# Optimization experiments

Hardware: AMD Instinct MI355X
Metric: run time of the kernel (lower is better)

The kernel has to match this reference:

```python
import jax, jax.numpy as jnp
import numpy as np
from jax import lax

# dims: B batch, C=d_model=256, IMG=128, P=4 patch, H=W=32, L=H*W=1024
# D=d_inner=512 (ssm_ratio 2.0), N=d_state=16, R=dt_rank=16, K=4 scan directions
B, C, IMG, P = 2, 256, 128, 4
H = W = IMG // P
L = H * W
D_INNER, N, R, K = 512, 16, 16, 4


def layernorm(x, g, b, eps=1e-5):
    mu = jnp.mean(x, axis=-1, keepdims=True)
    var = jnp.var(x, axis=-1, keepdims=True)
    return (x - mu) * lax.rsqrt(var + eps) * g + b


def setup_inputs() -> dict:
    key = jax.random.key(0)
    ks = jax.random.split(key, 12)
    f = lambda i, shape, s=0.02: jax.random.normal(ks[i], shape, jnp.float32) * s
    A_init = jnp.tile(jnp.arange(1, N + 1, dtype=jnp.float32)[None, None, :], (K, D_INNER, 1))
    return {
        "x": jax.random.normal(ks[0], (B, C, IMG, IMG), jnp.float32),
        "patch_w": f(1, (C, C, P, P)),
        "patch_b": jnp.zeros((C,), jnp.float32),
        "ln_g": jnp.ones((C,), jnp.float32),
        "ln_b": jnp.zeros((C,), jnp.float32),
        "in_w": f(2, (2 * D_INNER, C)),
        "conv_w": f(3, (D_INNER, 1, 3, 3)),
        "conv_b": jnp.zeros((D_INNER,), jnp.float32),
        "xproj_w": f(4, (K, R + 2 * N, D_INNER)),
        "dt_w": f(5, (K, D_INNER, R)),
        "dt_b": f(6, (K, D_INNER), 0.1),
        "A_log": jnp.log(A_init),
        "Ds": jnp.ones((K, D_INNER), jnp.float32),
        "on_g": jnp.ones((D_INNER,), jnp.float32),
        "on_b": jnp.zeros((D_INNER,), jnp.float32),
        "out_w": f(7, (C, D_INNER)),
        "head_w": f(8, (1, C)),
        "head_b": jnp.zeros((1,), jnp.float32),
    }


def _forward(x, patch_w, patch_b, ln_g, ln_b, in_w, conv_w, conv_b, xproj_w,
             dt_w, dt_b, A_log, Ds, on_g, on_b, out_w, head_w, head_b):
    dn = ("NCHW", "OIHW", "NCHW")
    # GRL is identity in forward. Patch embed conv, stride = patch.
    t = lax.conv_general_dilated(x, patch_w, (P, P), "VALID", dimension_numbers=dn)
    t = t + patch_b[None, :, None, None]
    t = jnp.transpose(t, (0, 2, 3, 1))                      # (B,H,W,C)

    # ---- VSS block: t + SS2D(LN(t)) ----
    u = layernorm(t, ln_g, ln_b)
    xz = jnp.einsum("bhwc,ec->bhwe", u, in_w)               # (B,H,W,2D)
    xc, z = jnp.split(xz, 2, axis=-1)
    xc = jnp.transpose(xc, (0, 3, 1, 2))                    # (B,D,H,W)
    xc = lax.conv_general_dilated(xc, conv_w, (1, 1), "SAME",
                                  dimension_numbers=dn, feature_group_count=D_INNER)
    xc = jax.nn.silu(xc + conv_b[None, :, None, None])

    # cross-scan: row-major, col-major, and their reverses -> (B,K,D,L)
    x_hw = xc.reshape(B, D_INNER, L)
    x_wh = jnp.transpose(xc, (0, 1, 3, 2)).reshape(B, D_INNER, L)
    xs = jnp.stack([x_hw, x_wh], axis=1)
    xs = jnp.concatenate([xs, jnp.flip(xs, axis=-1)], axis=1)  # (B,4,D,L)

    x_dbl = jnp.einsum("bkdl,kcd->bkcl", xs, xproj_w)          # (B,K,R+2N,L)
    dts_r = x_dbl[:, :, :R]
    Bs = x_dbl[:, :, R:R + N]                                  # (B,K,N,L)
    Cs = x_dbl[:, :, R + N:]                                   # (B,K,N,L)
    dts = jnp.einsum("bkrl,kdr->bkdl", dts_r, dt_w) + dt_b[None, :, :, None]
    dts = jax.nn.softplus(dts)                                 # (B,K,D,L)

    A = -jnp.exp(A_log)                                        # (K,D,N)
    dA = jnp.exp(dts[:, :, :, None, :] * A[None, :, :, :, None])      # (B,K,D,N,L)
    dBu = (dts * xs)[:, :, :, None, :] * Bs[:, :, None, :, :]         # (B,K,D,N,L)

    dA_t = jnp.moveaxis(dA, -1, 0)        # (L,B,K,D,N)
    dBu_t = jnp.moveaxis(dBu, -1, 0)
    Cs_t = jnp.moveaxis(Cs, -1, 0)        # (L,B,K,N)

    def step(h, inputs):
        dA_i, dBu_i, C_i = inputs
        h = dA_i * h + dBu_i
        y = jnp.einsum("bkdn,bkn->bkd", h, C_i)
        return h, y

    h0 = jnp.zeros((B, K, D_INNER, N), xs.dtype)
    _, ys = lax.scan(step, h0, (dA_t, dBu_t, Cs_t))           # ys: (L,B,K,D)
    ys = jnp.moveaxis(ys, 0, -1)                               # (B,K,D,L)
    ys = ys + Ds[None, :, :, None] * xs

    # cross-merge (invert the 4 scan orders and sum)
    y_rev = jnp.flip(ys[:, 2:], axis=-1)                        # (B,2,D,L)
    y_hw = ys[:, 0] + y_rev[:, 0]
    y_wh = ys[:, 1] + y_rev[:, 1]
    y_wh = jnp.transpose(y_wh.reshape(B, D_INNER, W, H), (0, 1, 3, 2)).reshape(B, D_INNER, L)
    y = (y_hw + y_wh).reshape(B, D_INNER, H, W)
    y = jnp.transpose(y, (0, 2, 3, 1))                          # (B,H,W,D)

    y = layernorm(y, on_g, on_b) * jax.nn.silu(z)
    ss_out = jnp.einsum("bhwd,cd->bhwc", y, out_w)
    t = t + ss_out

    # global average pool + head
    pooled = jnp.mean(t, axis=(1, 2))                           # (B,C)
    return pooled @ head_w.T + head_b


def reference(x, patch_w, patch_b, ln_g, ln_b, in_w, conv_w, conv_b, xproj_w,
              dt_w, dt_b, A_log, Ds, on_g, on_b, out_w, head_w, head_b):
    return _forward(x, patch_w, patch_b, ln_g, ln_b, in_w, conv_w, conv_b, xproj_w,
                    dt_w, dt_b, A_log, Ds, on_g, on_b, out_w, head_w, head_b)
```

## Files before the change

### kernel.cpp

```cpp
#include <hip/hip_runtime.h>
#include <math.h>


typedef __attribute__((ext_vector_type(4))) float f32x4;
typedef __attribute__((ext_vector_type(8))) short bf16x8;

__device__ __forceinline__ ushort bf16_rn(float f) {
  uint u = __float_as_uint(f);
  return (ushort)((u + 0x7fffu + ((u >> 16) & 1u)) >> 16);
}
__device__ __forceinline__ float bf2f(uint us) { return __uint_as_float(us << 16); }
__device__ __forceinline__ uint packbf(float a, float b) {
  return (uint)bf16_rn(a) | ((uint)bf16_rn(b) << 16);
}

__global__ __launch_bounds__(256) void prep_kernel(const float* __restrict__ x,
    ushort* __restrict__ Ap,
    const float* __restrict__ pw, const float* __restrict__ iw,
    const float* __restrict__ ow, const float* __restrict__ xw,
    const float* __restrict__ hw,
    ushort* __restrict__ pwh,
    ushort* __restrict__ iwh, ushort* __restrict__ iwl,
    ushort* __restrict__ xwh, ushort* __restrict__ xwl,
    float* __restrict__ weff) {
  int bid = blockIdx.x;
  int tid = threadIdx.x;
  if (bid < 2048) {
    __shared__ __align__(16) ushort tile[32][136];
    int b = bid >> 10, hh = (bid >> 5) & 31, c0 = (bid & 31) * 8;
    int ci = tid >> 5, ph = (tid >> 3) & 3, w4 = tid & 7;
    const float* src = x + (((long)(b * 256 + c0 + ci) * 128 + 4 * hh + ph) * 128 + 16 * w4);
    #pragma unroll
    for (int j = 0; j < 4; ++j) {
      float4 v = *(const float4*)(src + 4 * j);
      uint2 pk;
      pk.x = packbf(v.x, v.y);
      pk.y = packbf(v.z, v.w);
      *(uint2*)&tile[w4 * 4 + j][ci * 16 + ph * 4] = pk;
    }
    __syncthreads();
    int w = tid >> 3;
    long rowbase = ((long)(b * 1024 + hh * 32 + w)) * 4096 + c0 * 16;
    #pragma unroll
    for (int i = 0; i < 2; ++i) {
      int gr = (tid & 7) + 8 * i;
      *(uint4*)&Ap[rowbase + gr * 8] = *(const uint4*)&tile[w][gr * 8];
    }
  } else {
    int i = (bid - 2048) * 256 + tid;
    if (i < 1048576) {
      pwh[i] = bf16_rn(pw[i]);
      return;
    }
    if (i < 1409024) {
      const float* src; ushort* hi; ushort* lo; int off;
      if (i < 1310720) { src = iw; hi = iwh; lo = iwl; off = i - 1048576; }
      else             { src = xw; hi = xwh; lo = xwl; off = i - 1310720; }
      float f = src[off];
      ushort h = bf16_rn(f);
      hi[off] = h;
      lo[off] = bf16_rn(f - __uint_as_float(((uint)h) << 16));
      return;
    }
    if (i < 1409536) {
      int k = i - 1409024;
      float s = 0.f;
      #pragma unroll 8
      for (int c = 0; c < 256; ++c) s += ow[c * 512 + k] * hw[c];
      weff[k] = s;
    }
  }
}

__global__ __launch_bounds__(512) void mfma_bf(
    const ushort* __restrict__ A, const ushort* __restrict__ Bhi,
    const ushort* __restrict__ Blo, float* __restrict__ Cout, float* __restrict__ C2,
    int M, int N, int K, int kchunk, int mode, int NBM, int NBZ, int uselo)
{
  __shared__ __align__(16) ushort Ah[128 * 64];
  __shared__ __align__(16) ushort Bh[64 * 64];
  __shared__ __align__(16) ushort Bl[64 * 64];
  int tid = threadIdx.x;
  int bid = blockIdx.x;
  int kz = bid % NBZ;
  int n0 = (bid / (NBZ * NBM)) * 64;
  int m0 = ((bid / NBZ) % NBM) * 128;
  int k0 = kz * kchunk;
  int wid = tid >> 6, lane = tid & 63;
  int wm = wid >> 1, wn = wid & 1;
  int lrow = lane & 15, g = lane >> 4;
  f32x4 acc[2][2] = {};
  int nkt = kchunk >> 6;
  for (int kt = 0; kt < nkt; ++kt) {
    int kb = k0 + (kt << 6);
    {
      int gi = tid & 7;
      #pragma unroll
      for (int i = 0; i < 2; ++i) {
        int row = (tid >> 3) + (i << 6);
        uint4 v = *(const uint4*)&A[(long)(m0 + row) * K + kb + gi * 8];
        *(uint4*)&Ah[row * 64 + ((gi ^ (row & 7)) << 3)] = v;
      }
      int row = tid >> 3;
      long off = (long)(n0 + row) * K + kb + gi * 8;
      int la = row * 64 + ((gi ^ (row & 7)) << 3);
      *(uint4*)&Bh[la] = *(const uint4*)&Bhi[off];
      if (uselo) *(uint4*)&Bl[la] = *(const uint4*)&Blo[off];
    }
    __syncthreads();
    #pragma unroll
    for (int kk = 0; kk < 2; ++kk) {
      bf16x8 af[2], bhf[2];
      #pragma unroll
      for (int mi = 0; mi < 2; ++mi) {
        int row = wm * 32 + mi * 16 + lrow;
        af[mi] = *(const bf16x8*)&Ah[row * 64 + ((((kk << 2) + g) ^ (row & 7)) << 3)];
      }
      #pragma unroll
      for (int ni = 0; ni < 2; ++ni) {
        int row = wn * 32 + ni * 16 + lrow;
        int col = (((kk << 2) + g) ^ (row & 7)) << 3;
        bhf[ni] = *(const bf16x8*)&Bh[row * 64 + col];
      }
      #pragma unroll
      for (int mi = 0; mi < 2; ++mi)
        #pragma unroll
        for (int ni = 0; ni < 2; ++ni)
          acc[mi][ni] = __builtin_amdgcn_mfma_f32_16x16x32_bf16(af[mi], bhf[ni], acc[mi][ni], 0, 0, 0);
      if (uselo) {
        #pragma unroll
        for (int ni = 0; ni < 2; ++ni) {
          int row = wn * 32 + ni * 16 + lrow;
          int col = (((kk << 2) + g) ^ (row & 7)) << 3;
          bf16x8 blf = *(const bf16x8*)&Bl[row * 64 + col];
          #pragma unroll
          for (int mi = 0; mi < 2; ++mi)
            acc[mi][ni] = __builtin_amdgcn_mfma_f32_16x16x32_bf16(af[mi], blf, acc[mi][ni], 0, 0, 0);
        }
      }
    }
    __syncthreads();
  }
  int r4 = lane >> 4;
  if (mode == 2) {
    bool xhalf = (n0 < 512);
    ushort* xcb = (ushort*)Cout;
    #pragma unroll
    for (int mi = 0; mi < 2; ++mi)
      #pragma unroll
      for (int ni = 0; ni < 2; ++ni) {
        int n = n0 + wn * 32 + ni * 16 + lrow;
        int mb = m0 + wm * 32 + mi * 16 + r4 * 4;
        int bb = mb >> 10, l = mb & 1023;
        if (xhalf) {
          uint2 o;
          o.x = packbf(acc[mi][ni][0], acc[mi][ni][1]);
          o.y = packbf(acc[mi][ni][2], acc[mi][ni][3]);
          *(uint2*)&xcb[((long)(bb * 512 + n)) * 1024 + l] = o;
        } else {
          #pragma unroll
          for (int r = 0; r < 4; ++r)
            C2[(long)(mb + r) * 512 + (n - 512)] = acc[mi][ni][r];
        }
      }
  } else {
    long zoff = (long)kz * M * N;
    #pragma unroll
    for (int mi = 0; mi < 2; ++mi)
      #pragma unroll
      for (int ni = 0; ni < 2; ++ni) {
        int n = n0 + wn * 32 + ni * 16 + lrow;
        int mb = m0 + wm * 32 + mi * 16 + r4 * 4;
        #pragma unroll
        for (int r = 0; r < 4; ++r)
          Cout[zoff + (long)(mb + r) * N + n] = acc[mi][ni][r];
      }
  }
}

__global__ __launch_bounds__(256) void mfma_x(
    const ushort* __restrict__ A, const ushort* __restrict__ Bhi,
    const ushort* __restrict__ Blo, float* __restrict__ xdbl)
{
  __shared__ __align__(16) ushort Ah[64 * 64];
  __shared__ __align__(16) ushort Bh[48 * 64];
  __shared__ __align__(16) ushort Bl[48 * 64];
  int tid = threadIdx.x;
  int m0 = blockIdx.x * 64;
  int z = blockIdx.y, k = z & 3;
  const ushort* Az = A + (long)z * 524288;
  const ushort* Bhz = Bhi + (long)k * 24576;
  const ushort* Blz = Blo + (long)k * 24576;
  int lane = tid & 63, wv = tid >> 6;
  int lrow = lane & 15, g = lane >> 4;
  f32x4 acc[3] = {};
  for (int kt = 0; kt < 8; ++kt) {
    int kb = kt << 6;
    #pragma unroll
    for (int i = 0; i < 2; ++i) {
      int idx = i * 256 + tid;
      int row = idx >> 3, gi = idx & 7;
      uint4 v = *(const uint4*)&Az[(long)(m0 + row) * 512 + kb + gi * 8];
      *(uint4*)&Ah[row * 64 + ((gi ^ (row & 7)) << 3)] = v;
      if (idx < 384) {
        long off = (long)row * 512 + kb + gi * 8;
        int la = row * 64 + ((gi ^ (row & 7)) << 3);
        *(uint4*)&Bh[la] = *(const uint4*)&Bhz[off];
        *(uint4*)&Bl[la] = *(const uint4*)&Blz[off];
      }
    }
    __syncthreads();
    #pragma unroll
    for (int kk = 0; kk < 2; ++kk) {
      int arow = wv * 16 + lrow;
      bf16x8 af = *(const bf16x8*)&Ah[arow * 64 + ((((kk << 2) + g) ^ (arow & 7)) << 3)];
      #pragma unroll
      for (int ni = 0; ni < 3; ++ni) {
        int brow = ni * 16 + lrow;
        int col = (((kk << 2) + g) ^ (brow & 7)) << 3;
        bf16x8 bh = *(const bf16x8*)&Bh[brow * 64 + col];
        bf16x8 bl = *(const bf16x8*)&Bl[brow * 64 + col];
        acc[ni] = __builtin_amdgcn_mfma_f32_16x16x32_bf16(af, bh, acc[ni], 0, 0, 0);
        acc[ni] = __builtin_amdgcn_mfma_f32_16x16x32_bf16(af, bl, acc[ni], 0, 0, 0);
      }
    }
    __syncthreads();
  }
  float* Cz = xdbl + (long)z * 49152;
  int r4 = lane >> 4;
  #pragma unroll
  for (int ni = 0; ni < 3; ++ni) {
    int n = ni * 16 + lrow;
    int mb = m0 + wv * 16 + r4 * 4;
    #pragma unroll
    for (int r = 0; r < 4; ++r)
      Cz[(long)(mb + r) * 48 + n] = acc[ni][r];
  }
}

__device__ __forceinline__ float blk_sum(float v, float* sm) {
  #pragma unroll
  for (int o = 32; o > 0; o >>= 1) v += __shfl_down(v, o);
  int wid = threadIdx.x >> 6, lane = threadIdx.x & 63;
  __syncthreads();
  if (lane == 0) sm[wid] = v;
  __syncthreads();
  int nw = blockDim.x >> 6;
  float r = 0.f;
  for (int i = 0; i < nw; ++i) r += sm[i];
  return r;
}

__global__ __launch_bounds__(256) void reduce_ln1(const float* __restrict__ P,
    const float* __restrict__ bias, const float* __restrict__ g,
    const float* __restrict__ b, ushort* __restrict__ u,
    const float* __restrict__ hw, float* __restrict__ tpart) {
  __shared__ float sm[8];
  int m = blockIdx.x, c = threadIdx.x;
  float v = bias[c];
  #pragma unroll
  for (int s = 0; s < 8; ++s) v += P[(long)s * 524288 + m * 256 + c];
  float s1 = blk_sum(v, sm);
  float s2 = blk_sum(v * v, sm);
  float s3 = blk_sum(v * hw[c], sm);
  if (c == 0) tpart[m] = s3;
  float mu = s1 * (1.f / 256.f);
  float var = s2 * (1.f / 256.f) - mu * mu;
  float rs = rsqrtf(var + 1e-5f);
  u[(long)m * 256 + c] = bf16_rn((v - mu) * rs * g[c] + b[c]);
}

__global__ __launch_bounds__(256) void head_final(const float* __restrict__ tpart,
    const float* __restrict__ spart, const float* __restrict__ hb,
    float* __restrict__ out) {
  __shared__ float sm[8];
  int b = blockIdx.x, tid = threadIdx.x;
  float s = 0.f;
  #pragma unroll
  for (int j = 0; j < 4; ++j) {
    int m = b * 1024 + tid * 4 + j;
    s += tpart[m] + spart[m];
  }
  float tot = blk_sum(s, sm);
  if (tid == 0) out[b] = tot * (1.f / 1024.f) + hb[0];
}

__global__ __launch_bounds__(256) void dwconv_kernel(const ushort* __restrict__ xc,
    const float* __restrict__ cw, const float* __restrict__ cb, ushort* __restrict__ out) {
  __shared__ float plane[32][33];
  int d = blockIdx.x, b = blockIdx.y;
  long base = ((long)b * 512 + d) * 1024;
  int tid = threadIdx.x;
  uint2 v = *(const uint2*)&xc[base + tid * 4];
  int h0 = (tid * 4) >> 5, w0 = (tid * 4) & 31;
  plane[h0][w0 + 0] = bf2f(v.x & 0xffff); plane[h0][w0 + 1] = bf2f(v.x >> 16);
  plane[h0][w0 + 2] = bf2f(v.y & 0xffff); plane[h0][w0 + 3] = bf2f(v.y >> 16);
  float w9[9];
  #pragma unroll
  for (int i = 0; i < 9; ++i) w9[i] = cw[d * 9 + i];
  float bias = cb[d];
  __syncthreads();
  float o4[4];
  #pragma unroll
  for (int j = 0; j < 4; ++j) {
    int p = tid * 4 + j, h = p >> 5, w = p & 31;
    float acc = 0.f;
    #pragma unroll
    for (int dh = -1; dh <= 1; ++dh) {
      int hy = h + dh;
      if (hy < 0 || hy > 31) continue;
      #pragma unroll
      for (int dw = -1; dw <= 1; ++dw) {
        int wx = w + dw;
        if (wx < 0 || wx > 31) continue;
        acc += w9[(dh + 1) * 3 + (dw + 1)] * plane[hy][wx];
      }
    }
    acc += bias;
    o4[j] = acc / (1.f + __expf(-acc));
  }
  uint2 o2;
  o2.x = packbf(o4[0], o4[1]);
  o2.y = packbf(o4[2], o4[3]);
  *(uint2*)&out[base + tid * 4] = o2;
}

__global__ __launch_bounds__(256) void build_xsT(const ushort* __restrict__ xca,
    ushort* __restrict__ xsTb) {
  __shared__ ushort tile[32][34];
  int h = blockIdx.x;
  int d0 = blockIdx.y * 32;
  int z = blockIdx.z;
  int b = z >> 2, k = z & 3;
  int tid = threadIdx.x;
  int a = tid >> 5, q = tid & 31;
  #pragma unroll
  for (int i = 0; i < 4; ++i) {
    int di = a + i * 8;
    tile[di][q] = xca[((long)(b * 512 + d0 + di)) * 1024 + h * 32 + q];
  }
  __syncthreads();
  #pragma unroll
  for (int i = 0; i < 4; ++i) {
    int w = a + i * 8;
    int r;
    if (k == 0) r = h * 32 + w;
    else if (k == 1) r = w * 32 + h;
    else if (k == 2) r = 1023 - (h * 32 + w);
    else r = 1023 - (w * 32 + h);
    xsTb[((long)z * 1024 + r) * 512 + d0 + q] = tile[q][w];
  }
}

template<bool FINAL>
__global__ __launch_bounds__(128) void scan_chunk6(
    const float* __restrict__ xdbl, ushort* xsb,
    const float* __restrict__ dtw, const float* __restrict__ dtb,
    const float* __restrict__ A_log, const float* __restrict__ Ds,
    float* __restrict__ dsum, float* __restrict__ hpb)
{
  __shared__ float sdt[32][64];
  __shared__ float sxv[16][64];
  __shared__ float sy[16][64];
  __shared__ float sBC[32][32];
  float (*sR)[16] = (float(*)[16])sy;
  int tid = threadIdx.x;
  int dl = tid >> 1, ng = tid & 1;
  int d0 = blockIdx.x * 64;
  int d = d0 + dl;
  int c = blockIdx.y;
  int z = blockIdx.z;
  int k = z & 3;
  long baseD = (long)z * 524288;
  int l0 = c * 32;
  const float* xdz = xdbl + (long)z * 49152 + (long)l0 * 48;
  #pragma unroll
  for (int i = 0; i < 2; ++i) {
    int idx = i * 128 + tid;
    int l = idx >> 3, q = idx & 7;
    *(float4*)&sBC[l][q * 4] = *(const float4*)(xdz + l * 48 + 16 + q * 4);
  }
  {
    int l = tid >> 2, q = tid & 3;
    *(float4*)&sR[l][q * 4] = *(const float4*)(xdz + l * 48 + q * 4);
  }
  float a[8], h[8];
  #pragma unroll
  for (int j = 0; j < 8; ++j) {
    a[j] = -__expf(A_log[((long)k * 512 + d) * 16 + ng * 8 + j]);
    h[j] = 0.f;
  }
  float4 wr0 = *(const float4*)(dtw + ((long)k * 512 + d) * 16);
  float4 wr1 = *(const float4*)(dtw + ((long)k * 512 + d) * 16 + 4);
  float4 wr2 = *(const float4*)(dtw + ((long)k * 512 + d) * 16 + 8);
  float4 wr3 = *(const float4*)(dtw + ((long)k * 512 + d) * 16 + 12);
  float dbias = dtb[k * 512 + d];
  int gbase = c * 65536 + z * 8192 + d * 16 + ng * 8;
  float Dv = 0.f;
  if (FINAL) {
    #pragma unroll
    for (int j = 0; j < 8; ++j) h[j] = hpb[gbase + j];
    Dv = Ds[k * 512 + d];
  }
  __syncthreads();
  #pragma unroll
  for (int li = 0; li < 16; ++li) {
    int l = ng * 16 + li;
    const float* rr = &sR[l][0];
    float acc = dbias;
    acc += wr0.x * rr[0];  acc += wr0.y * rr[1];  acc += wr0.z * rr[2];  acc += wr0.w * rr[3];
    acc += wr1.x * rr[4];  acc += wr1.y * rr[5];  acc += wr1.z * rr[6];  acc += wr1.w * rr[7];
    acc += wr2.x * rr[8];  acc += wr2.y * rr[9];  acc += wr2.z * rr[10]; acc += wr2.w * rr[11];
    acc += wr3.x * rr[12]; acc += wr3.y * rr[13]; acc += wr3.z * rr[14]; acc += wr3.w * rr[15];
    sdt[l][dl] = (acc > 20.f) ? acc : __logf(1.f + __expf(acc));
  }
  __syncthreads();
  int xli = tid >> 3;
  int xdj = (tid & 7) * 8;
  uint4 rxv = *(const uint4*)&xsb[baseD + (long)(l0 + xli) * 512 + d0 + xdj];
  float dtsum = 0.f;
  for (int t = 0; t < 2; ++t) {
    {
      float4 f0, f1;
      f0.x = bf2f(rxv.x & 0xffff); f0.y = bf2f(rxv.x >> 16);
      f0.z = bf2f(rxv.y & 0xffff); f0.w = bf2f(rxv.y >> 16);
      f1.x = bf2f(rxv.z & 0xffff); f1.y = bf2f(rxv.z >> 16);
      f1.z = bf2f(rxv.w & 0xffff); f1.w = bf2f(rxv.w >> 16);
      *(float4*)&sxv[xli][xdj] = f0;
      *(float4*)&sxv[xli][xdj + 4] = f1;
    }
    __syncthreads();
    if (t == 0)
      rxv = *(const uint4*)&xsb[baseD + (long)(l0 + 16 + xli) * 512 + d0 + xdj];
    #pragma unroll
    for (int li = 0; li < 16; ++li) {
      int lr = t * 16 + li;
      float dt = sdt[lr][dl];
      float xv = sxv[li][dl];
      float w = dt * xv;
      float4 B0 = *(const float4*)&sBC[lr][ng * 8];
      float4 B1 = *(const float4*)&sBC[lr][ng * 8 + 4];
      if (!FINAL) {
        dtsum += dt;
        h[0] = __expf(dt * a[0]) * h[0] + w * B0.x;
        h[1] = __expf(dt * a[1]) * h[1] + w * B0.y;
        h[2] = __expf(dt * a[2]) * h[2] + w * B0.z;
        h[3] = __expf(dt * a[3]) * h[3] + w * B0.w;
        h[4] = __expf(dt * a[4]) * h[4] + w * B1.x;
        h[5] = __expf(dt * a[5]) * h[5] + w * B1.y;
        h[6] = __expf(dt * a[6]) * h[6] + w * B1.z;
        h[7] = __expf(dt * a[7]) * h[7] + w * B1.w;
      } else {
        float4 C0 = *(const float4*)&sBC[lr][16 + ng * 8];
        float4 C1 = *(const float4*)&sBC[lr][16 + ng * 8 + 4];
        float p;
        h[0] = __expf(dt * a[0]) * h[0] + w * B0.x; p  = h[0] * C0.x;
        h[1] = __expf(dt * a[1]) * h[1] + w * B0.y; p += h[1] * C0.y;
        h[2] = __expf(dt * a[2]) * h[2] + w * B0.z; p += h[2] * C0.z;
        h[3] = __expf(dt * a[3]) * h[3] + w * B0.w; p += h[3] * C0.w;
        h[4] = __expf(dt * a[4]) * h[4] + w * B1.x; p += h[4] * C1.x;
        h[5] = __expf(dt * a[5]) * h[5] + w * B1.y; p += h[5] * C1.y;
        h[6] = __expf(dt * a[6]) * h[6] + w * B1.z; p += h[6] * C1.z;
        h[7] = __expf(dt * a[7]) * h[7] + w * B1.w; p += h[7] * C1.w;
        p += __shfl_xor(p, 1);
        if (ng == 0) sy[li][dl] = p + Dv * xv;
      }
    }
    __syncthreads();
    if (FINAL) {
      float4 f0 = *(float4*)&sy[xli][xdj];
      float4 f1 = *(float4*)&sy[xli][xdj + 4];
      uint4 o;
      o.x = packbf(f0.x, f0.y); o.y = packbf(f0.z, f0.w);
      o.z = packbf(f1.x, f1.y); o.w = packbf(f1.z, f1.w);
      *(uint4*)&xsb[baseD + (long)(l0 + t * 16 + xli) * 512 + d0 + xdj] = o;
    }
  }
  if (!FINAL) {
    *(float4*)(hpb + gbase)     = make_float4(h[0], h[1], h[2], h[3]);
    *(float4*)(hpb + gbase + 4) = make_float4(h[4], h[5], h[6], h[7]);
    if (ng == 0) dsum[c * 4096 + z * 512 + d] = dtsum;
  }
}

__global__ __launch_bounds__(256) void scan_prefix(const float* __restrict__ dsum,
    const float* __restrict__ A_log, float* __restrict__ hpb) {
  int g = blockIdx.x * 256 + threadIdx.x;
  int z = g >> 13, n = g & 15;
  int d = (g >> 4) & 511;
  int k = z & 3;
  float a = -__expf(A_log[((long)k * 512 + d) * 16 + n]);
  float h = 0.f;
  #pragma unroll
  for (int c = 0; c < 32; ++c) {
    float P = __expf(dsum[c * 4096 + z * 512 + d] * a);
    float hp = hpb[c * 65536 + g];
    hpb[c * 65536 + g] = h;
    h = P * h + hp;
  }
}

__global__ __launch_bounds__(256) void combine_ln2gate(const ushort* __restrict__ ys,
    const float* __restrict__ zb, const float* __restrict__ g,
    const float* __restrict__ b, const float* __restrict__ weff,
    float* __restrict__ spart) {
  __shared__ float sm[8];
  int m = blockIdx.x, tid = threadIdx.x;
  int bb = m >> 10, l = m & 1023;
  int hh = l >> 5, w = l & 31;
  int lw = w * 32 + hh;
  long b4 = (long)bb * 4;
  uint u0 = *(const uint*)&ys[((b4 + 0) * 1024 + l) * 512 + tid * 2];
  uint u1 = *(const uint*)&ys[((b4 + 2) * 1024 + (1023 - l)) * 512 + tid * 2];
  uint u2 = *(const uint*)&ys[((b4 + 1) * 1024 + lw) * 512 + tid * 2];
  uint u3 = *(const uint*)&ys[((b4 + 3) * 1024 + (1023 - lw)) * 512 + tid * 2];
  float v0 = bf2f(u0 & 0xffff) + bf2f(u1 & 0xffff) + bf2f(u2 & 0xffff) + bf2f(u3 & 0xffff);
  float v1 = bf2f(u0 >> 16) + bf2f(u1 >> 16) + bf2f(u2 >> 16) + bf2f(u3 >> 16);
  float s1 = blk_sum(v0 + v1, sm);
  float s2 = blk_sum(v0 * v0 + v1 * v1, sm);
  float mu = s1 * (1.f / 512.f);
  float var = s2 * (1.f / 512.f) - mu * mu;
  float rs = rsqrtf(var + 1e-5f);
  float2 gg = *(const float2*)(g + tid * 2);
  float2 bbv = *(const float2*)(b + tid * 2);
  float2 zz = *(const float2*)(zb + (long)m * 512 + tid * 2);
  float y0 = ((v0 - mu) * rs * gg.x + bbv.x) * (zz.x / (1.f + __expf(-zz.x)));
  float y1 = ((v1 - mu) * rs * gg.y + bbv.y) * (zz.y / (1.f + __expf(-zz.y)));
  float2 we = *(const float2*)(weff + tid * 2);
  float s3 = blk_sum(y0 * we.x + y1 * we.y, sm);
  if (tid == 0) spart[m] = s3;
}

extern "C" void kernel_launch(void* const* d_in, const int* in_sizes, int n_in,
                              void* d_out, int out_size, void* d_ws, size_t ws_size,
                              hipStream_t stream) {
  const float* x       = (const float*)d_in[0];
  const float* patch_w = (const float*)d_in[1];
  const float* patch_b = (const float*)d_in[2];
  const float* ln_g    = (const float*)d_in[3];
  const float* ln_b    = (const float*)d_in[4];
  const float* in_w    = (const float*)d_in[5];
  const float* conv_w  = (const float*)d_in[6];
  const float* conv_b  = (const float*)d_in[7];
  const float* xproj_w = (const float*)d_in[8];
  const float* dt_w    = (const float*)d_in[9];
  const float* dt_b    = (const float*)d_in[10];
  const float* A_log   = (const float*)d_in[11];
  const float* Ds      = (const float*)d_in[12];
  const float* on_g    = (const float*)d_in[13];
  const float* on_b    = (const float*)d_in[14];
  const float* out_w   = (const float*)d_in[15];
  const float* head_w  = (const float*)d_in[16];
  const float* head_b  = (const float*)d_in[17];

  float* ws = (float*)d_ws;
  float* t_buf   = ws;
  float* u_buf   = t_buf + 524288;
  float* xz_buf  = u_buf + 524288;
  float* xc_buf  = xz_buf + 2097152;
  float* xca_buf = xc_buf + 1048576;
  float* xsT_buf = xca_buf + 1048576;
  float* xdbl_buf= xsT_buf + 4194304;
  float* spl_buf = xdbl_buf + 393216;
  float* tail    = spl_buf + 4194304;
  float*  tpart  = t_buf;
  float*  spart  = t_buf + 2048;
  ushort* A_p    = (ushort*)xsT_buf;
  ushort* pw_hi  = (ushort*)xz_buf;
  float*  z_buf  = xz_buf;
  float*  P_patch= spl_buf;
  ushort* u_bf   = (ushort*)u_buf;
  ushort* xc_bf  = (ushort*)xc_buf;
  ushort* xca_bf = (ushort*)xca_buf;
  ushort* iw_hi  = (ushort*)tail;
  ushort* iw_lo  = (ushort*)(tail + 131072);
  ushort* xw_hi  = (ushort*)(tail + 262144);
  ushort* xw_lo  = (ushort*)(tail + 311296);
  float*  weff_buf = tail + 360448;
  ushort* xsT_bf = (ushort*)(tail + 360960);
  float*  dsum_buf = tail + 2458112;
  float*  hp_buf   = tail + 2589184;

  prep_kernel<<<7554, 256, 0, stream>>>(x, A_p, patch_w, in_w, out_w, xproj_w,
      head_w, pw_hi, iw_hi, iw_lo, xw_hi, xw_lo, weff_buf);
  mfma_bf<<<512, 512, 0, stream>>>(A_p, pw_hi, nullptr, P_patch, nullptr,
      2048, 256, 4096, 512, 0, 16, 8, 0);
  reduce_ln1<<<2048, 256, 0, stream>>>(P_patch, patch_b, ln_g, ln_b, u_bf,
      head_w, tpart);
  mfma_bf<<<256, 512, 0, stream>>>(u_bf, iw_hi, iw_lo, xc_buf, z_buf,
      2048, 1024, 256, 256, 2, 16, 1, 1);
  dwconv_kernel<<<dim3(512, 2), 256, 0, stream>>>(xc_bf, conv_w, conv_b, xca_bf);
  build_xsT<<<dim3(32, 16, 8), 256, 0, stream>>>(xca_bf, xsT_bf);
  mfma_x<<<dim3(16, 8), 256, 0, stream>>>(xsT_bf, xw_hi, xw_lo, xdbl_buf);
  scan_chunk6<false><<<dim3(8, 32, 8), 128, 0, stream>>>(xdbl_buf, xsT_bf,
      dt_w, dt_b, A_log, Ds, dsum_buf, hp_buf);
  scan_prefix<<<256, 256, 0, stream>>>(dsum_buf, A_log, hp_buf);
  scan_chunk6<true><<<dim3(8, 32, 8), 128, 0, stream>>>(xdbl_buf, xsT_bf,
      dt_w, dt_b, A_log, Ds, nullptr, hp_buf);
  combine_ln2gate<<<2048, 256, 0, stream>>>(xsT_bf, z_buf, on_g, on_b,
      weff_buf, spart);
  head_final<<<2, 256, 0, stream>>>(tpart, spart, head_b, (float*)d_out);
}
```

Measured before the change: 132.1 us.

## Fuse input/weight bf16 conversion into GEMM loads and merge block reductions

Removes the separate prep kernel that converted the input image into a patch-major bf16 matrix and pre-split the weights into bf16 hi/lo parts. The GEMM kernels now read fp32 input and weights directly and convert them while staging into shared memory, with the patch gather done inline. The ln reductions are also merged into multi-value block sums to cut synchronisations. This trades one full round trip of the input through memory for redundant weight conversion in every block and uncoalesced strided fp32 loads in the patch GEMM.

```diff
diff --git a/kernel.cpp b/kernel.cpp
--- a/kernel.cpp
+++ b/kernel.cpp
@@ -14,68 +14,20 @@
   return (uint)bf16_rn(a) | ((uint)bf16_rn(b) << 16);
 }
 
-__global__ __launch_bounds__(256) void prep_kernel(const float* __restrict__ x,
-    ushort* __restrict__ Ap,
-    const float* __restrict__ pw, const float* __restrict__ iw,
-    const float* __restrict__ ow, const float* __restrict__ xw,
-    const float* __restrict__ hw,
-    ushort* __restrict__ pwh,
-    ushort* __restrict__ iwh, ushort* __restrict__ iwl,
-    ushort* __restrict__ xwh, ushort* __restrict__ xwl,
-    float* __restrict__ weff) {
-  int bid = blockIdx.x;
-  int tid = threadIdx.x;
-  if (bid < 2048) {
-    __shared__ __align__(16) ushort tile[32][136];
-    int b = bid >> 10, hh = (bid >> 5) & 31, c0 = (bid & 31) * 8;
-    int ci = tid >> 5, ph = (tid >> 3) & 3, w4 = tid & 7;
-    const float* src = x + (((long)(b * 256 + c0 + ci) * 128 + 4 * hh + ph) * 128 + 16 * w4);
-    #pragma unroll
-    for (int j = 0; j < 4; ++j) {
-      float4 v = *(const float4*)(src + 4 * j);
-      uint2 pk;
-      pk.x = packbf(v.x, v.y);
-      pk.y = packbf(v.z, v.w);
-      *(uint2*)&tile[w4 * 4 + j][ci * 16 + ph * 4] = pk;
-    }
-    __syncthreads();
-    int w = tid >> 3;
-    long rowbase = ((long)(b * 1024 + hh * 32 + w)) * 4096 + c0 * 16;
-    #pragma unroll
-    for (int i = 0; i < 2; ++i) {
-      int gr = (tid & 7) + 8 * i;
-      *(uint4*)&Ap[rowbase + gr * 8] = *(const uint4*)&tile[w][gr * 8];
-    }
-  } else {
-    int i = (bid - 2048) * 256 + tid;
-    if (i < 1048576) {
-      pwh[i] = bf16_rn(pw[i]);
-      return;
-    }
-    if (i < 1409024) {
-      const float* src; ushort* hi; ushort* lo; int off;
-      if (i < 1310720) { src = iw; hi = iwh; lo = iwl; off = i - 1048576; }
-      else             { src = xw; hi = xwh; lo = xwl; off = i - 1310720; }
-      float f = src[off];
-      ushort h = bf16_rn(f);
-      hi[off] = h;
-      lo[off] = bf16_rn(f - __uint_as_float(((uint)h) << 16));
-      return;
-    }
-    if (i < 1409536) {
-      int k = i - 1409024;
-      float s = 0.f;
-      #pragma unroll 8
-      for (int c = 0; c < 256; ++c) s += ow[c * 512 + k] * hw[c];
-      weff[k] = s;
-    }
-  }
-}
-
+__global__ __launch_bounds__(256) void weff_kernel(const float* __restrict__ ow,
+    const float* __restrict__ hw, float* __restrict__ weff) {
+  int k = blockIdx.x * 256 + threadIdx.x;
+  float s = 0.f;
+  #pragma unroll 8
+  for (int c = 0; c < 256; ++c) s += ow[c * 512 + k] * hw[c];
+  weff[k] = s;
+}
+
+template<int MODE, bool PATCH, bool USELO>
 __global__ __launch_bounds__(512) void mfma_bf(
-    const ushort* __restrict__ A, const ushort* __restrict__ Bhi,
-    const ushort* __restrict__ Blo, float* __restrict__ Cout, float* __restrict__ C2,
-    int M, int N, int K, int kchunk, int mode, int NBM, int NBZ, int uselo)
+    const void* __restrict__ Ain, const float* __restrict__ Bf,
+    float* __restrict__ Cout, float* __restrict__ C2,
+    int M, int N, int K, int kchunk, int NBM, int NBZ)
 {
   __shared__ __align__(16) ushort Ah[128 * 64];
   __shared__ __align__(16) ushort Bh[64 * 64];
@@ -93,19 +45,52 @@
   int nkt = kchunk >> 6;
   for (int kt = 0; kt < nkt; ++kt) {
     int kb = k0 + (kt << 6);
-    {
-      int gi = tid & 7;
+    int gi = tid & 7;
+    if (PATCH) {
+      const float* X = (const float*)Ain;
       #pragma unroll
       for (int i = 0; i < 2; ++i) {
         int row = (tid >> 3) + (i << 6);
-        uint4 v = *(const uint4*)&A[(long)(m0 + row) * K + kb + gi * 8];
+        int m = m0 + row, bb = m >> 10, l = m & 1023, hh = l >> 5, w = l & 31;
+        int kg = kb + gi * 8;
+        int ci = kg >> 4, ph = (kg >> 2) & 3;
+        const float* s0 = X + (((long)(bb * 256 + ci) * 128 + 4 * hh + ph) * 128 + 4 * w);
+        float4 va = *(const float4*)s0;
+        float4 vb = *(const float4*)(s0 + 128);
+        uint4 o;
+        o.x = packbf(va.x, va.y); o.y = packbf(va.z, va.w);
+        o.z = packbf(vb.x, vb.y); o.w = packbf(vb.z, vb.w);
+        *(uint4*)&Ah[row * 64 + ((gi ^ (row & 7)) << 3)] = o;
+      }
+    } else {
+      const ushort* Abf = (const ushort*)Ain;
+      #pragma unroll
+      for (int i = 0; i < 2; ++i) {
+        int row = (tid >> 3) + (i << 6);
+        uint4 v = *(const uint4*)&Abf[(long)(m0 + row) * K + kb + gi * 8];
         *(uint4*)&Ah[row * 64 + ((gi ^ (row & 7)) << 3)] = v;
       }
+    }
+    {
       int row = tid >> 3;
       long off = (long)(n0 + row) * K + kb + gi * 8;
+      float4 w0 = *(const float4*)(Bf + off);
+      float4 w1 = *(const float4*)(Bf + off + 4);
       int la = row * 64 + ((gi ^ (row & 7)) << 3);
-      *(uint4*)&Bh[la] = *(const uint4*)&Bhi[off];
-      if (uselo) *(uint4*)&Bl[la] = *(const uint4*)&Blo[off];
+      ushort h0 = bf16_rn(w0.x), h1 = bf16_rn(w0.y), h2 = bf16_rn(w0.z), h3 = bf16_rn(w0.w);
+      ushort h4 = bf16_rn(w1.x), h5 = bf16_rn(w1.y), h6 = bf16_rn(w1.z), h7 = bf16_rn(w1.w);
+      uint4 oh;
+      oh.x = (uint)h0 | ((uint)h1 << 16); oh.y = (uint)h2 | ((uint)h3 << 16);
+      oh.z = (uint)h4 | ((uint)h5 << 16); oh.w = (uint)h6 | ((uint)h7 << 16);
+      *(uint4*)&Bh[la] = oh;
+      if (USELO) {
+        uint4 ol;
+        ol.x = packbf(w0.x - bf2f(h0), w0.y - bf2f(h1));
+        ol.y = packbf(w0.z - bf2f(h2), w0.w - bf2f(h3));
+        ol.z = packbf(w1.x - bf2f(h4), w1.y - bf2f(h5));
+        ol.w = packbf(w1.z - bf2f(h6), w1.w - bf2f(h7));
+        *(uint4*)&Bl[la] = ol;
+      }
     }
     __syncthreads();
     #pragma unroll
@@ -127,7 +112,7 @@
         #pragma unroll
         for (int ni = 0; ni < 2; ++ni)
           acc[mi][ni] = __builtin_amdgcn_mfma_f32_16x16x32_bf16(af[mi], bhf[ni], acc[mi][ni], 0, 0, 0);
-      if (uselo) {
+      if (USELO) {
         #pragma unroll
         for (int ni = 0; ni < 2; ++ni) {
           int row = wn * 32 + ni * 16 + lrow;
@@ -142,7 +127,7 @@
     __syncthreads();
   }
   int r4 = lane >> 4;
-  if (mode == 2) {
+  if (MODE == 2) {
     bool xhalf = (n0 < 512);
     ushort* xcb = (ushort*)Cout;
     #pragma unroll
@@ -179,8 +164,8 @@
 }
 
 __global__ __launch_bounds__(256) void mfma_x(
-    const ushort* __restrict__ A, const ushort* __restrict__ Bhi,
-    const ushort* __restrict__ Blo, float* __restrict__ xdbl)
+    const ushort* __restrict__ A, const float* __restrict__ XW,
+    float* __restrict__ xdbl)
 {
   __shared__ __align__(16) ushort Ah[64 * 64];
   __shared__ __align__(16) ushort Bh[48 * 64];
@@ -189,8 +174,7 @@
   int m0 = blockIdx.x * 64;
   int z = blockIdx.y, k = z & 3;
   const ushort* Az = A + (long)z * 524288;
-  const ushort* Bhz = Bhi + (long)k * 24576;
-  const ushort* Blz = Blo + (long)k * 24576;
+  const float* Bz = XW + (long)k * 24576;
   int lane = tid & 63, wv = tid >> 6;
   int lrow = lane & 15, g = lane >> 4;
   f32x4 acc[3] = {};
@@ -204,9 +188,21 @@
       *(uint4*)&Ah[row * 64 + ((gi ^ (row & 7)) << 3)] = v;
       if (idx < 384) {
         long off = (long)row * 512 + kb + gi * 8;
+        float4 w0 = *(const float4*)(Bz + off);
+        float4 w1 = *(const float4*)(Bz + off + 4);
         int la = row * 64 + ((gi ^ (row & 7)) << 3);
-        *(uint4*)&Bh[la] = *(const uint4*)&Bhz[off];
-        *(uint4*)&Bl[la] = *(const uint4*)&Blz[off];
+        ushort h0 = bf16_rn(w0.x), h1 = bf16_rn(w0.y), h2 = bf16_rn(w0.z), h3 = bf16_rn(w0.w);
+        ushort h4 = bf16_rn(w1.x), h5 = bf16_rn(w1.y), h6 = bf16_rn(w1.z), h7 = bf16_rn(w1.w);
+        uint4 oh;
+        oh.x = (uint)h0 | ((uint)h1 << 16); oh.y = (uint)h2 | ((uint)h3 << 16);
+        oh.z = (uint)h4 | ((uint)h5 << 16); oh.w = (uint)h6 | ((uint)h7 << 16);
+        *(uint4*)&Bh[la] = oh;
+        uint4 ol;
+        ol.x = packbf(w0.x - bf2f(h0), w0.y - bf2f(h1));
+        ol.y = packbf(w0.z - bf2f(h2), w0.w - bf2f(h3));
+        ol.z = packbf(w1.x - bf2f(h4), w1.y - bf2f(h5));
+        ol.w = packbf(w1.z - bf2f(h6), w1.w - bf2f(h7));
+        *(uint4*)&Bl[la] = ol;
       }
     }
     __syncthreads();
@@ -245,24 +241,43 @@
   __syncthreads();
   if (lane == 0) sm[wid] = v;
   __syncthreads();
-  int nw = blockDim.x >> 6;
-  float r = 0.f;
-  for (int i = 0; i < nw; ++i) r += sm[i];
-  return r;
+  return sm[0] + sm[1] + sm[2] + sm[3];
+}
+__device__ __forceinline__ void blk_sum2(float& a, float& b, float* sm) {
+  #pragma unroll
+  for (int o = 32; o > 0; o >>= 1) { a += __shfl_down(a, o); b += __shfl_down(b, o); }
+  int wid = threadIdx.x >> 6, lane = threadIdx.x & 63;
+  __syncthreads();
+  if (lane == 0) { sm[wid * 2] = a; sm[wid * 2 + 1] = b; }
+  __syncthreads();
+  a = sm[0] + sm[2] + sm[4] + sm[6];
+  b = sm[1] + sm[3] + sm[5] + sm[7];
+}
+__device__ __forceinline__ void blk_sum3(float& a, float& b, float& c, float* sm) {
+  #pragma unroll
+  for (int o = 32; o > 0; o >>= 1) {
+    a += __shfl_down(a, o); b += __shfl_down(b, o); c += __shfl_down(c, o);
+  }
+  int wid = threadIdx.x >> 6, lane = threadIdx.x & 63;
+  __syncthreads();
+  if (lane == 0) { sm[wid * 3] = a; sm[wid * 3 + 1] = b; sm[wid * 3 + 2] = c; }
+  __syncthreads();
+  a = sm[0] + sm[3] + sm[6] + sm[9];
+  b = sm[1] + sm[4] + sm[7] + sm[10];
+  c = sm[2] + sm[5] + sm[8] + sm[11];
 }
 
 __global__ __launch_bounds__(256) void reduce_ln1(const float* __restrict__ P,
     const float* __restrict__ bias, const float* __restrict__ g,
     const float* __restrict__ b, ushort* __restrict__ u,
     const float* __restrict__ hw, float* __restrict__ tpart) {
-  __shared__ float sm[8];
+  __shared__ float sm[12];
   int m = blockIdx.x, c = threadIdx.x;
   float v = bias[c];
   #pragma unroll
   for (int s = 0; s < 8; ++s) v += P[(long)s * 524288 + m * 256 + c];
-  float s1 = blk_sum(v, sm);
-  float s2 = blk_sum(v * v, sm);
-  float s3 = blk_sum(v * hw[c], sm);
+  float s1 = v, s2 = v * v, s3 = v * hw[c];
+  blk_sum3(s1, s2, s3, sm);
   if (c == 0) tpart[m] = s3;
   float mu = s1 * (1.f / 256.f);
   float var = s2 * (1.f / 256.f) - mu * mu;
@@ -273,7 +288,7 @@
 __global__ __launch_bounds__(256) void head_final(const float* __restrict__ tpart,
     const float* __restrict__ spart, const float* __restrict__ hb,
     float* __restrict__ out) {
-  __shared__ float sm[8];
+  __shared__ float sm[4];
   int b = blockIdx.x, tid = threadIdx.x;
   float s = 0.f;
   #pragma unroll
@@ -516,8 +531,8 @@
   uint u3 = *(const uint*)&ys[((b4 + 3) * 1024 + (1023 - lw)) * 512 + tid * 2];
   float v0 = bf2f(u0 & 0xffff) + bf2f(u1 & 0xffff) + bf2f(u2 & 0xffff) + bf2f(u3 & 0xffff);
   float v1 = bf2f(u0 >> 16) + bf2f(u1 >> 16) + bf2f(u2 >> 16) + bf2f(u3 >> 16);
-  float s1 = blk_sum(v0 + v1, sm);
-  float s2 = blk_sum(v0 * v0 + v1 * v1, sm);
+  float s1 = v0 + v1, s2 = v0 * v0 + v1 * v1;
+  blk_sum2(s1, s2, sm);
   float mu = s1 * (1.f / 512.f);
   float var = s2 * (1.f / 512.f) - mu * mu;
   float rs = rsqrtf(var + 1e-5f);
@@ -554,44 +569,29 @@
   const float* head_b  = (const float*)d_in[17];
 
   float* ws = (float*)d_ws;
-  float* t_buf   = ws;
-  float* u_buf   = t_buf + 524288;
-  float* xz_buf  = u_buf + 524288;
-  float* xc_buf  = xz_buf + 2097152;
-  float* xca_buf = xc_buf + 1048576;
-  float* xsT_buf = xca_buf + 1048576;
-  float* xdbl_buf= xsT_buf + 4194304;
-  float* spl_buf = xdbl_buf + 393216;
-  float* tail    = spl_buf + 4194304;
-  float*  tpart  = t_buf;
-  float*  spart  = t_buf + 2048;
-  ushort* A_p    = (ushort*)xsT_buf;
-  ushort* pw_hi  = (ushort*)xz_buf;
-  float*  z_buf  = xz_buf;
-  float*  P_patch= spl_buf;
-  ushort* u_bf   = (ushort*)u_buf;
-  ushort* xc_bf  = (ushort*)xc_buf;
-  ushort* xca_bf = (ushort*)xca_buf;
-  ushort* iw_hi  = (ushort*)tail;
-  ushort* iw_lo  = (ushort*)(tail + 131072);
-  ushort* xw_hi  = (ushort*)(tail + 262144);
-  ushort* xw_lo  = (ushort*)(tail + 311296);
-  float*  weff_buf = tail + 360448;
-  ushort* xsT_bf = (ushort*)(tail + 360960);
-  float*  dsum_buf = tail + 2458112;
-  float*  hp_buf   = tail + 2589184;
-
-  prep_kernel<<<7554, 256, 0, stream>>>(x, A_p, patch_w, in_w, out_w, xproj_w,
-      head_w, pw_hi, iw_hi, iw_lo, xw_hi, xw_lo, weff_buf);
-  mfma_bf<<<512, 512, 0, stream>>>(A_p, pw_hi, nullptr, P_patch, nullptr,
-      2048, 256, 4096, 512, 0, 16, 8, 0);
+  float*  tpart   = ws;
+  float*  spart   = ws + 2048;
+  float*  weff_buf= ws + 4096;
+  float*  z_buf   = ws + 8192;
+  ushort* u_bf    = (ushort*)(ws + 1056768);
+  ushort* xc_bf   = (ushort*)(ws + 1318912);
+  ushort* xca_bf  = (ushort*)(ws + 1843200);
+  ushort* xsT_bf  = (ushort*)(ws + 2367488);
+  float*  xdbl_buf= ws + 4464640;
+  float*  P_patch = ws + 4857856;
+  float*  dsum_buf= ws + 9052160;
+  float*  hp_buf  = ws + 9183232;
+
+  weff_kernel<<<2, 256, 0, stream>>>(out_w, head_w, weff_buf);
+  mfma_bf<0, true, false><<<512, 512, 0, stream>>>(x, patch_w, P_patch, nullptr,
+      2048, 256, 4096, 512, 16, 8);
   reduce_ln1<<<2048, 256, 0, stream>>>(P_patch, patch_b, ln_g, ln_b, u_bf,
       head_w, tpart);
-  mfma_bf<<<256, 512, 0, stream>>>(u_bf, iw_hi, iw_lo, xc_buf, z_buf,
-      2048, 1024, 256, 256, 2, 16, 1, 1);
+  mfma_bf<2, false, true><<<256, 512, 0, stream>>>(u_bf, in_w, (float*)xc_bf, z_buf,
+      2048, 1024, 256, 256, 16, 1);
   dwconv_kernel<<<dim3(512, 2), 256, 0, stream>>>(xc_bf, conv_w, conv_b, xca_bf);
   build_xsT<<<dim3(32, 16, 8), 256, 0, stream>>>(xca_bf, xsT_bf);
-  mfma_x<<<dim3(16, 8), 256, 0, stream>>>(xsT_bf, xw_hi, xw_lo, xdbl_buf);
+  mfma_x<<<dim3(16, 8), 256, 0, stream>>>(xsT_bf, xproj_w, xdbl_buf);
   scan_chunk6<false><<<dim3(8, 32, 8), 128, 0, stream>>>(xdbl_buf, xsT_bf,
       dt_w, dt_b, A_log, Ds, dsum_buf, hp_buf);
   scan_prefix<<<256, 256, 0, stream>>>(dsum_buf, A_log, hp_buf);
```

After: 134.6 us. No clear change (+1.9%).

## Fuse depthwise conv into scan-layout build, batch block reductions, halve split-K

Applied to the files above, without the earlier changes.

Merges the depthwise 3x3 conv+SiLU kernel into the kernel that builds the four transposed scan layouts. Each block recomputes the conv for its row using a 3-row halo, so the intermediate activation is never written to and reread from memory and one launch is removed. Block reductions in the two layernorm kernels now reduce two or three values in a single pass with fewer barriers. The patch-embed GEMM goes from split-K 8 to split-K 4, which halves the partial sums reduce_ln1 must read at the cost of fewer blocks, and the workspace layout is repacked. The fused kernel repeats the conv work across the 4 scan directions and the halo reads.

```diff
diff --git a/kernel.cpp b/kernel.cpp
--- a/kernel.cpp
+++ b/kernel.cpp
@@ -245,24 +245,43 @@
   __syncthreads();
   if (lane == 0) sm[wid] = v;
   __syncthreads();
-  int nw = blockDim.x >> 6;
-  float r = 0.f;
-  for (int i = 0; i < nw; ++i) r += sm[i];
-  return r;
+  return sm[0] + sm[1] + sm[2] + sm[3];
+}
+__device__ __forceinline__ void blk_sum2(float& a, float& b, float* sm) {
+  #pragma unroll
+  for (int o = 32; o > 0; o >>= 1) { a += __shfl_down(a, o); b += __shfl_down(b, o); }
+  int wid = threadIdx.x >> 6, lane = threadIdx.x & 63;
+  __syncthreads();
+  if (lane == 0) { sm[wid * 2] = a; sm[wid * 2 + 1] = b; }
+  __syncthreads();
+  a = sm[0] + sm[2] + sm[4] + sm[6];
+  b = sm[1] + sm[3] + sm[5] + sm[7];
+}
+__device__ __forceinline__ void blk_sum3(float& a, float& b, float& c, float* sm) {
+  #pragma unroll
+  for (int o = 32; o > 0; o >>= 1) {
+    a += __shfl_down(a, o); b += __shfl_down(b, o); c += __shfl_down(c, o);
+  }
+  int wid = threadIdx.x >> 6, lane = threadIdx.x & 63;
+  __syncthreads();
+  if (lane == 0) { sm[wid * 3] = a; sm[wid * 3 + 1] = b; sm[wid * 3 + 2] = c; }
+  __syncthreads();
+  a = sm[0] + sm[3] + sm[6] + sm[9];
+  b = sm[1] + sm[4] + sm[7] + sm[10];
+  c = sm[2] + sm[5] + sm[8] + sm[11];
 }
 
 __global__ __launch_bounds__(256) void reduce_ln1(const float* __restrict__ P,
     const float* __restrict__ bias, const float* __restrict__ g,
     const float* __restrict__ b, ushort* __restrict__ u,
     const float* __restrict__ hw, float* __restrict__ tpart) {
-  __shared__ float sm[8];
+  __shared__ float sm[12];
   int m = blockIdx.x, c = threadIdx.x;
   float v = bias[c];
   #pragma unroll
-  for (int s = 0; s < 8; ++s) v += P[(long)s * 524288 + m * 256 + c];
-  float s1 = blk_sum(v, sm);
-  float s2 = blk_sum(v * v, sm);
-  float s3 = blk_sum(v * hw[c], sm);
+  for (int s = 0; s < 4; ++s) v += P[(long)s * 524288 + m * 256 + c];
+  float s1 = v, s2 = v * v, s3 = v * hw[c];
+  blk_sum3(s1, s2, s3, sm);
   if (c == 0) tpart[m] = s3;
   float mu = s1 * (1.f / 256.f);
   float var = s2 * (1.f / 256.f) - mu * mu;
@@ -273,7 +292,7 @@
 __global__ __launch_bounds__(256) void head_final(const float* __restrict__ tpart,
     const float* __restrict__ spart, const float* __restrict__ hb,
     float* __restrict__ out) {
-  __shared__ float sm[8];
+  __shared__ float sm[4];
   int b = blockIdx.x, tid = threadIdx.x;
   float s = 0.f;
   #pragma unroll
@@ -285,61 +304,49 @@
   if (tid == 0) out[b] = tot * (1.f / 1024.f) + hb[0];
 }
 
-__global__ __launch_bounds__(256) void dwconv_kernel(const ushort* __restrict__ xc,
-    const float* __restrict__ cw, const float* __restrict__ cb, ushort* __restrict__ out) {
-  __shared__ float plane[32][33];
-  int d = blockIdx.x, b = blockIdx.y;
-  long base = ((long)b * 512 + d) * 1024;
-  int tid = threadIdx.x;
-  uint2 v = *(const uint2*)&xc[base + tid * 4];
-  int h0 = (tid * 4) >> 5, w0 = (tid * 4) & 31;
-  plane[h0][w0 + 0] = bf2f(v.x & 0xffff); plane[h0][w0 + 1] = bf2f(v.x >> 16);
-  plane[h0][w0 + 2] = bf2f(v.y & 0xffff); plane[h0][w0 + 3] = bf2f(v.y >> 16);
-  float w9[9];
-  #pragma unroll
-  for (int i = 0; i < 9; ++i) w9[i] = cw[d * 9 + i];
-  float bias = cb[d];
-  __syncthreads();
-  float o4[4];
-  #pragma unroll
-  for (int j = 0; j < 4; ++j) {
-    int p = tid * 4 + j, h = p >> 5, w = p & 31;
-    float acc = 0.f;
-    #pragma unroll
-    for (int dh = -1; dh <= 1; ++dh) {
-      int hy = h + dh;
-      if (hy < 0 || hy > 31) continue;
-      #pragma unroll
-      for (int dw = -1; dw <= 1; ++dw) {
-        int wx = w + dw;
-        if (wx < 0 || wx > 31) continue;
-        acc += w9[(dh + 1) * 3 + (dw + 1)] * plane[hy][wx];
-      }
-    }
-    acc += bias;
-    o4[j] = acc / (1.f + __expf(-acc));
-  }
-  uint2 o2;
-  o2.x = packbf(o4[0], o4[1]);
-  o2.y = packbf(o4[2], o4[3]);
-  *(uint2*)&out[base + tid * 4] = o2;
-}
-
-__global__ __launch_bounds__(256) void build_xsT(const ushort* __restrict__ xca,
+__global__ __launch_bounds__(256) void dwbuild(const ushort* __restrict__ xc,
+    const float* __restrict__ cw, const float* __restrict__ cb,
     ushort* __restrict__ xsTb) {
+  __shared__ float pl[3][32][33];
   __shared__ ushort tile[32][34];
   int h = blockIdx.x;
   int d0 = blockIdx.y * 32;
   int z = blockIdx.z;
   int b = z >> 2, k = z & 3;
   int tid = threadIdx.x;
+  int dd = tid >> 3, w4 = (tid & 7) * 4;
+  #pragma unroll
+  for (int r = 0; r < 3; ++r) {
+    int hh = h - 1 + r;
+    float4 vv = make_float4(0.f, 0.f, 0.f, 0.f);
+    if (hh >= 0 && hh < 32) {
+      uint2 v = *(const uint2*)&xc[((long)(b * 512 + d0 + dd)) * 1024 + hh * 32 + w4];
+      vv.x = bf2f(v.x & 0xffff); vv.y = bf2f(v.x >> 16);
+      vv.z = bf2f(v.y & 0xffff); vv.w = bf2f(v.y >> 16);
+    }
+    pl[r][dd][w4] = vv.x; pl[r][dd][w4 + 1] = vv.y;
+    pl[r][dd][w4 + 2] = vv.z; pl[r][dd][w4 + 3] = vv.w;
+  }
+  float w9[9];
+  #pragma unroll
+  for (int i = 0; i < 9; ++i) w9[i] = cw[(d0 + dd) * 9 + i];
+  float bias = cb[d0 + dd];
+  __syncthreads();
+  #pragma unroll
+  for (int j = 0; j < 4; ++j) {
+    int w = w4 + j;
+    float acc = 0.f;
+    #pragma unroll
+    for (int r = 0; r < 3; ++r) {
+      if (w > 0)  acc += w9[r * 3 + 0] * pl[r][dd][w - 1];
+      acc += w9[r * 3 + 1] * pl[r][dd][w];
+      if (w < 31) acc += w9[r * 3 + 2] * pl[r][dd][w + 1];
+    }
+    acc += bias;
+    tile[dd][w] = bf16_rn(acc / (1.f + __expf(-acc)));
+  }
+  __syncthreads();
   int a = tid >> 5, q = tid & 31;
-  #pragma unroll
-  for (int i = 0; i < 4; ++i) {
-    int di = a + i * 8;
-    tile[di][q] = xca[((long)(b * 512 + d0 + di)) * 1024 + h * 32 + q];
-  }
-  __syncthreads();
   #pragma unroll
   for (int i = 0; i < 4; ++i) {
     int w = a + i * 8;
@@ -516,8 +523,8 @@
   uint u3 = *(const uint*)&ys[((b4 + 3) * 1024 + (1023 - lw)) * 512 + tid * 2];
   float v0 = bf2f(u0 & 0xffff) + bf2f(u1 & 0xffff) + bf2f(u2 & 0xffff) + bf2f(u3 & 0xffff);
   float v1 = bf2f(u0 >> 16) + bf2f(u1 >> 16) + bf2f(u2 >> 16) + bf2f(u3 >> 16);
-  float s1 = blk_sum(v0 + v1, sm);
-  float s2 = blk_sum(v0 * v0 + v1 * v1, sm);
+  float s1 = v0 + v1, s2 = v0 * v0 + v1 * v1;
+  blk_sum2(s1, s2, sm);
   float mu = s1 * (1.f / 512.f);
   float var = s2 * (1.f / 512.f) - mu * mu;
   float rs = rsqrtf(var + 1e-5f);
@@ -554,43 +561,33 @@
   const float* head_b  = (const float*)d_in[17];
 
   float* ws = (float*)d_ws;
-  float* t_buf   = ws;
-  float* u_buf   = t_buf + 524288;
-  float* xz_buf  = u_buf + 524288;
-  float* xc_buf  = xz_buf + 2097152;
-  float* xca_buf = xc_buf + 1048576;
-  float* xsT_buf = xca_buf + 1048576;
-  float* xdbl_buf= xsT_buf + 4194304;
-  float* spl_buf = xdbl_buf + 393216;
-  float* tail    = spl_buf + 4194304;
-  float*  tpart  = t_buf;
-  float*  spart  = t_buf + 2048;
-  ushort* A_p    = (ushort*)xsT_buf;
-  ushort* pw_hi  = (ushort*)xz_buf;
-  float*  z_buf  = xz_buf;
-  float*  P_patch= spl_buf;
-  ushort* u_bf   = (ushort*)u_buf;
-  ushort* xc_bf  = (ushort*)xc_buf;
-  ushort* xca_bf = (ushort*)xca_buf;
-  ushort* iw_hi  = (ushort*)tail;
-  ushort* iw_lo  = (ushort*)(tail + 131072);
-  ushort* xw_hi  = (ushort*)(tail + 262144);
-  ushort* xw_lo  = (ushort*)(tail + 311296);
-  float*  weff_buf = tail + 360448;
-  ushort* xsT_bf = (ushort*)(tail + 360960);
-  float*  dsum_buf = tail + 2458112;
-  float*  hp_buf   = tail + 2589184;
+  float*  tpart   = ws;
+  float*  spart   = ws + 2048;
+  float*  weff_buf= ws + 4096;
+  float*  z_buf   = ws + 8192;
+  ushort* u_bf    = (ushort*)(ws + 1060864);
+  ushort* xc_bf   = (ushort*)(ws + 1323008);
+  ushort* xsT_bf  = (ushort*)(ws + 1847296);
+  float*  xdbl_buf= ws + 3944448;
+  float*  P_patch = ws + 4337664;
+  float*  dsum_buf= ws + 6434816;
+  float*  hp_buf  = ws + 6565888;
+  ushort* A_p     = (ushort*)(ws + 8663040);
+  ushort* pw_hi   = (ushort*)(ws + 12857344);
+  ushort* iw_hi   = (ushort*)(ws + 13381632);
+  ushort* iw_lo   = (ushort*)(ws + 13512704);
+  ushort* xw_hi   = (ushort*)(ws + 13643776);
+  ushort* xw_lo   = (ushort*)(ws + 13692928);
 
   prep_kernel<<<7554, 256, 0, stream>>>(x, A_p, patch_w, in_w, out_w, xproj_w,
       head_w, pw_hi, iw_hi, iw_lo, xw_hi, xw_lo, weff_buf);
-  mfma_bf<<<512, 512, 0, stream>>>(A_p, pw_hi, nullptr, P_patch, nullptr,
-      2048, 256, 4096, 512, 0, 16, 8, 0);
+  mfma_bf<<<256, 512, 0, stream>>>(A_p, pw_hi, nullptr, P_patch, nullptr,
+      2048, 256, 4096, 1024, 0, 16, 4, 0);
   reduce_ln1<<<2048, 256, 0, stream>>>(P_patch, patch_b, ln_g, ln_b, u_bf,
       head_w, tpart);
-  mfma_bf<<<256, 512, 0, stream>>>(u_bf, iw_hi, iw_lo, xc_buf, z_buf,
+  mfma_bf<<<256, 512, 0, stream>>>(u_bf, iw_hi, iw_lo, (float*)xc_bf, z_buf,
       2048, 1024, 256, 256, 2, 16, 1, 1);
-  dwconv_kernel<<<dim3(512, 2), 256, 0, stream>>>(xc_bf, conv_w, conv_b, xca_bf);
-  build_xsT<<<dim3(32, 16, 8), 256, 0, stream>>>(xca_bf, xsT_bf);
+  dwbuild<<<dim3(32, 16, 8), 256, 0, stream>>>(xc_bf, conv_w, conv_b, xsT_bf);
   mfma_x<<<dim3(16, 8), 256, 0, stream>>>(xsT_bf, xw_hi, xw_lo, xdbl_buf);
   scan_chunk6<false><<<dim3(8, 32, 8), 128, 0, stream>>>(xdbl_buf, xsT_bf,
       dt_w, dt_b, A_log, Ds, dsum_buf, hp_buf);
```

After: 133.2 us. About the same (+0.8%).
